# Kernel optimization log

Hardware: AMD Instinct MI355X
Metric: run time of the kernel (lower is better)

Reference implementation:

```python
import math
import jax, jax.numpy as jnp
import numpy as np

B, N, D, H = 4, 2048, 1024, 16
DK = D // H

def setup_inputs() -> dict:
    key = jax.random.key(0)
    k1, k2, k3 = jax.random.split(key, 3)
    x = jax.random.normal(k1, (B, N, D), dtype=jnp.float32)
    # torch Linear weight is [out,in]; we store transposed [in,out] for x @ W
    w_qkv = jax.random.normal(k2, (D, 3 * D), dtype=jnp.float32) * (1.0 / math.sqrt(D))
    w_out = jax.random.normal(k3, (D, D), dtype=jnp.float32) * (1.0 / math.sqrt(D))
    return {"x": x, "w_qkv": w_qkv, "w_out": w_out}

def reference(x, w_qkv, w_out):
    b, n, d = x.shape
    qkv = x @ w_qkv                                   # [B,N,3D]
    q, k, v = jnp.split(qkv, 3, axis=-1)
    def split_heads(t):
        return t.reshape(b, n, H, DK).transpose(0, 2, 1, 3)  # [B,H,N,DK]
    q, k, v = map(split_heads, (q, k, v))
    scale = 1.0 / math.sqrt(DK)
    attn = jnp.einsum('bhqd,bhkd->bhqk', q, k) * scale  # [B,H,N,N]
    attn = jax.nn.softmax(attn, axis=-1)
    out = jnp.einsum('bhqk,bhkd->bhqd', attn, v)        # [B,H,N,DK]
    out = out.transpose(0, 2, 1, 3).reshape(b, n, d)
    return out @ w_out                                  # dropout p=0 -> identity
```

## Files before the change

kernel.cpp:

```cpp
#include <hip/hip_runtime.h>
#include <hip/hip_bf16.h>

typedef __bf16 bf16;
typedef __bf16 bf16x8 __attribute__((ext_vector_type(8)));
typedef float f32x4 __attribute__((ext_vector_type(4)));
typedef float f32x16 __attribute__((ext_vector_type(16)));
typedef short s16x4 __attribute__((ext_vector_type(4)));

#define GLDS16(gp, lp) __builtin_amdgcn_global_load_lds( \
    (const __attribute__((address_space(1))) void*)(gp), \
    (__attribute__((address_space(3))) void*)(lp), 16, 0, 0)

__device__ __forceinline__ bf16 f2bf(float f) {
    unsigned u = __builtin_bit_cast(unsigned, f);
    u = (u + 0x7FFFu + ((u >> 16) & 1u)) >> 16;
    unsigned short s = (unsigned short)u;
    return __builtin_bit_cast(bf16, s);
}
__device__ __forceinline__ void store_c(float* p, float v) { *p = v; }
__device__ __forceinline__ void store_c(bf16*  p, float v) { *p = f2bf(v); }

__device__ __forceinline__ unsigned cvt_pk_bf16(float lo, float hi) {
    unsigned r;
    asm("v_cvt_pk_bf16_f32 %0, %1, %2" : "=v"(r) : "v"(lo), "v"(hi));
    return r;
}
__device__ __forceinline__ void permlane32_swap(unsigned &a, unsigned &b) {
    asm("v_permlane32_swap_b32 %0, %1" : "+v"(a), "+v"(b));
}
__device__ __forceinline__ s16x4 ds_tr16(unsigned addr) {
    s16x4 d;
    asm volatile("ds_read_b64_tr_b16 %0, %1" : "=v"(d) : "v"(addr));
    return d;
}

__global__ __launch_bounds__(256) void cvt_f32_bf16(
    const float* __restrict__ in, bf16* __restrict__ out, int n8)
{
    int i = blockIdx.x * 256 + threadIdx.x;
    if (i >= n8) return;
    f32x4 a = *(const f32x4*)(in + (size_t)i * 8);
    f32x4 b = *(const f32x4*)(in + (size_t)i * 8 + 4);
    bf16x8 o;
    #pragma unroll
    for (int j = 0; j < 4; ++j) { o[j] = f2bf(a[j]); o[4 + j] = f2bf(b[j]); }
    *(bf16x8*)(out + (size_t)i * 8) = o;
}

template <typename TC>
__global__ __launch_bounds__(256) void gemm_glds(
    const bf16* __restrict__ A, const bf16* __restrict__ B, TC* __restrict__ C,
    int M, int N, int K)
{
    __shared__ alignas(16) bf16 As[128 * 32];
    __shared__ alignas(16) bf16 Bs[32 * 128];

    const int tid  = threadIdx.x;
    const int wv   = tid >> 6;
    const int lane = tid & 63;
    const int lr   = lane & 15;
    const int kb   = lane >> 4;
    const int wr   = wv >> 1, wc = wv & 1;
    const int brow = blockIdx.y * 128;
    const int bcol = blockIdx.x * 128;

    f32x4 acc[4][4] = {};

    const int ar0 = wv * 16 + (lane >> 2);
    const int ac0 = (lane & 3) * 8;

    const int bL   = wv * 1024 + lane * 16;
    const int bs0  = bL >> 7;
    const int b_r  = (bL & 127) >> 5;
    const int b_c0 = (bL & 31) >> 1;

    for (int k0 = 0; k0 < K; k0 += 32) {
        __syncthreads();
        #pragma unroll
        for (int t = 0; t < 2; ++t)
            GLDS16(A + (size_t)(brow + t * 64 + ar0) * K + k0 + ac0,
                   &As[t * 2048 + wv * 512]);
        #pragma unroll
        for (int t = 0; t < 2; ++t) {
            int s = bs0 + t * 32;
            GLDS16(B + (size_t)(k0 + (s >> 3) * 4 + b_r) * N + bcol + (s & 7) * 16 + b_c0,
                   &Bs[t * 2048 + wv * 512]);
        }
        __syncthreads();

        bf16x8 af[4], bfr[4];
        #pragma unroll
        for (int m = 0; m < 4; ++m)
            af[m] = *(const bf16x8*)&As[(wr * 64 + m * 16 + lr) * 32 + kb * 8];
        {
            s16x4 tr[8];
            const unsigned bsb = (unsigned)(uintptr_t)Bs + kb * 2048 + lr * 8;
            #pragma unroll
            for (int nt = 0; nt < 4; ++nt) {
                unsigned a = bsb + (wc * 4 + nt) * 128;
                tr[nt * 2]     = ds_tr16(a);
                tr[nt * 2 + 1] = ds_tr16(a + 1024);
            }
            asm volatile("s_waitcnt lgkmcnt(0)" ::: "memory");
            __builtin_amdgcn_sched_barrier(0);
            #pragma unroll
            for (int nt = 0; nt < 4; ++nt) {
                union { bf16x8 f; s16x4 h[2]; } u;
                u.h[0] = tr[nt * 2]; u.h[1] = tr[nt * 2 + 1];
                bfr[nt] = u.f;
            }
        }
        #pragma unroll
        for (int m = 0; m < 4; ++m)
            #pragma unroll
            for (int n = 0; n < 4; ++n)
                acc[m][n] = __builtin_amdgcn_mfma_f32_16x16x32_bf16(af[m], bfr[n], acc[m][n], 0, 0, 0);
    }

    #pragma unroll
    for (int m = 0; m < 4; ++m)
        #pragma unroll
        for (int n = 0; n < 4; ++n)
            #pragma unroll
            for (int r = 0; r < 4; ++r) {
                int row = brow + wr * 64 + m * 16 + kb * 4 + r;
                int col = bcol + wc * 64 + n * 16 + lr;
                store_c(&C[(size_t)row * N + col], acc[m][n][r]);
            }
}

__global__ __launch_bounds__(256) void attn_mfma32(
    const bf16* __restrict__ qkv, bf16* __restrict__ attn_out)
{
    constexpr int NSEQ = 2048, DM = 1024, LD = 3072, KVB = 64, QB = 128;
    __shared__ alignas(16) char smem[18432];
    bf16 (*Ks)[72] = (bf16 (*)[72])smem;
    bf16 *Vs       = (bf16*)(smem + 9216);
    bf16 (*Os)[72] = (bf16 (*)[72])smem;

    const int tid = threadIdx.x;
    const int wv = tid >> 6, lane = tid & 63;
    const int l31 = lane & 31;
    const int hi_ = lane >> 5;
    const int g16 = (lane >> 4) & 1;
    const int l16 = lane & 15;
    const int q0 = blockIdx.x * QB;
    const int bh = blockIdx.y;
    const int b = bh >> 4, h = bh & 15;

    const bf16* qbase = qkv + (size_t)(b * NSEQ) * LD + h * 64;
    const bf16* kbase = qbase + DM;
    const bf16* vbase = qbase + 2 * DM;

    bf16x8 qf[4];
    {
        const bf16* qp = qbase + (size_t)(q0 + wv * 32 + l31) * LD + hi_ * 8;
        #pragma unroll
        for (int ds = 0; ds < 4; ++ds) {
            bf16x8 t = *(const bf16x8*)(qp + ds * 16);
            #pragma unroll
            for (int e = 0; e < 8; ++e) t[e] = f2bf((float)t[e] * 0.125f);
            qf[ds] = t;
        }
    }

    f32x16 o0 = {}, o1 = {};
    float mrow = -INFINITY, lsum = 0.f;

    const int krow = tid >> 2, kcol = (tid & 3) * 16;
    const unsigned vb = (unsigned)(uintptr_t)Vs;

    for (int kt = 0; kt < NSEQ / KVB; ++kt) {
        const int j0 = kt * KVB;
        bf16x8 kr0 = *(const bf16x8*)(kbase + (size_t)(j0 + krow) * LD + kcol);
        bf16x8 kr1 = *(const bf16x8*)(kbase + (size_t)(j0 + krow) * LD + kcol + 8);
        bf16x8 vr[2];
        #pragma unroll
        for (int w = 0; w < 2; ++w) {
            int L = w * 2048 + tid * 8;
            int kq = L >> 8, cb = (L >> 6) & 3, rr = (L >> 4) & 3, c0 = L & 15;
            vr[w] = *(const bf16x8*)(vbase + (size_t)(j0 + kq * 4 + rr) * LD + cb * 16 + c0);
        }
        __syncthreads();
        *(bf16x8*)&Ks[krow][kcol]       = kr0;
        *(bf16x8*)&Ks[krow][kcol + 8]   = kr1;
        *(bf16x8*)(Vs + tid * 8)        = vr[0];
        *(bf16x8*)(Vs + 2048 + tid * 8) = vr[1];
        __syncthreads();

        f32x16 sT0 = {}, sT1 = {};
        #pragma unroll
        for (int ds = 0; ds < 4; ++ds) {
            bf16x8 kf = *(const bf16x8*)&Ks[l31][ds * 16 + hi_ * 8];
            sT0 = __builtin_amdgcn_mfma_f32_32x32x16_bf16(kf, qf[ds], sT0, 0, 0, 0);
        }
        #pragma unroll
        for (int ds = 0; ds < 4; ++ds) {
            bf16x8 kf = *(const bf16x8*)&Ks[32 + l31][ds * 16 + hi_ * 8];
            sT1 = __builtin_amdgcn_mfma_f32_32x32x16_bf16(kf, qf[ds], sT1, 0, 0, 0);
        }

        float pm = sT0[0];
        #pragma unroll
        for (int r = 1; r < 16; ++r) pm = fmaxf(pm, sT0[r]);
        #pragma unroll
        for (int r = 0; r < 16; ++r) pm = fmaxf(pm, sT1[r]);
        pm = fmaxf(pm, __shfl_xor(pm, 32));
        const float mn = fmaxf(mrow, pm);
        const float corr = __expf(mrow - mn);
        mrow = mn;
        float ps = 0.f;
        #pragma unroll
        for (int r = 0; r < 16; ++r) { sT0[r] = __expf(sT0[r] - mn); ps += sT0[r]; }
        #pragma unroll
        for (int r = 0; r < 16; ++r) { sT1[r] = __expf(sT1[r] - mn); ps += sT1[r]; }
        ps += __shfl_xor(ps, 32);
        lsum = lsum * corr + ps;
        #pragma unroll
        for (int r = 0; r < 16; ++r) { o0[r] *= corr; o1[r] *= corr; }

        unsigned w0[8], w1[8];
        #pragma unroll
        for (int j = 0; j < 8; ++j) {
            w0[j] = cvt_pk_bf16(sT0[2 * j], sT0[2 * j + 1]);
            w1[j] = cvt_pk_bf16(sT1[2 * j], sT1[2 * j + 1]);
        }
        bf16x8 pf[4];
        #pragma unroll
        for (int ks = 0; ks < 4; ++ks) {
            const int jb = 4 * (ks & 1);
            unsigned a0 = (ks >> 1) ? w1[jb]     : w0[jb];
            unsigned b0 = (ks >> 1) ? w1[jb + 2] : w0[jb + 2];
            unsigned a1 = (ks >> 1) ? w1[jb + 1] : w0[jb + 1];
            unsigned b1 = (ks >> 1) ? w1[jb + 3] : w0[jb + 3];
            permlane32_swap(a0, b0);
            permlane32_swap(a1, b1);
            union { bf16x8 f; unsigned w[4]; } u;
            u.w[0] = a0; u.w[1] = a1; u.w[2] = b0; u.w[3] = b1;
            pf[ks] = u.f;
        }

        #pragma unroll
        for (int dt = 0; dt < 2; ++dt) {
            s16x4 t[8];
            #pragma unroll
            for (int ks = 0; ks < 4; ++ks) {
                unsigned a = vb + ks * 2048 + hi_ * 1024 + dt * 256 + g16 * 128 + l16 * 8;
                t[ks * 2]     = ds_tr16(a);
                t[ks * 2 + 1] = ds_tr16(a + 512);
            }
            asm volatile("s_waitcnt lgkmcnt(0)" ::: "memory");
            __builtin_amdgcn_sched_barrier(0);
            #pragma unroll
            for (int ks = 0; ks < 4; ++ks) {
                union { bf16x8 f; s16x4 h[2]; } u;
                u.h[0] = t[ks * 2]; u.h[1] = t[ks * 2 + 1];
                if (dt == 0) o0 = __builtin_amdgcn_mfma_f32_32x32x16_bf16(u.f, pf[ks], o0, 0, 0, 0);
                else         o1 = __builtin_amdgcn_mfma_f32_32x32x16_bf16(u.f, pf[ks], o1, 0, 0, 0);
            }
        }
    }

    const float inv = 1.f / lsum;
    __syncthreads();
    #pragma unroll
    for (int r = 0; r < 16; ++r) {
        const int d0 = (r & 3) + 8 * (r >> 2) + 4 * hi_;
        Os[wv * 32 + l31][d0]      = f2bf(o0[r] * inv);
        Os[wv * 32 + l31][32 + d0] = f2bf(o1[r] * inv);
    }
    __syncthreads();
    {
        const int row = tid >> 1, c0 = (tid & 1) * 32;
        bf16* op = attn_out + (size_t)(b * NSEQ + q0 + row) * DM + h * 64 + c0;
        #pragma unroll
        for (int e = 0; e < 4; ++e)
            *(bf16x8*)(op + e * 8) = *(const bf16x8*)&Os[row][c0 + e * 8];
    }
}

extern "C" void kernel_launch(void* const* d_in, const int* in_sizes, int n_in,
                              void* d_out, int out_size, void* d_ws, size_t ws_size,
                              hipStream_t stream) {
    const float* x     = (const float*)d_in[0];
    const float* w_qkv = (const float*)d_in[1];
    const float* w_out = (const float*)d_in[2];
    float* out = (float*)d_out;

    bf16* x_bf    = (bf16*)d_out;
    bf16* qkv     = (bf16*)d_ws;
    bf16* wqkv_bf = qkv + (size_t)8192 * 3072;
    bf16* attnb   = wqkv_bf;
    bf16* wo_bf   = (bf16*)d_ws;

    cvt_f32_bf16<<<4096, 256, 0, stream>>>(x, x_bf, 8192 * 1024 / 8);
    cvt_f32_bf16<<<1536, 256, 0, stream>>>(w_qkv, wqkv_bf, 1024 * 3072 / 8);
    gemm_glds<bf16><<<dim3(3072 / 128, 8192 / 128), 256, 0, stream>>>(
        x_bf, wqkv_bf, qkv, 8192, 3072, 1024);
    attn_mfma32<<<dim3(2048 / 128, 64), 256, 0, stream>>>(qkv, attnb);
    cvt_f32_bf16<<<512, 256, 0, stream>>>(w_out, wo_bf, 1024 * 1024 / 8);
    gemm_glds<float><<<dim3(1024 / 128, 8192 / 128), 256, 0, stream>>>(
        attnb, wo_bf, out, 8192, 1024, 1024);
}
```

Baseline: 240.5 us.

## Prefetch next K/V tile into registers, use exp2 and lazy softmax rescale

The attention kernel now issues global loads for the next K/V tile right after the LDS stores, so they overlap with the current tile's MFMA and softmax work. Q is prescaled by log2(e), which lets the exponentials use the raw v_exp_f32 instruction. The running-max rescale of the accumulators is skipped unless some lane's new max exceeds the old one by more than a threshold. MFMA sections are also bracketed with s_setprio. This trades extra registers for the prefetch and risks bf16 overflow or precision loss from the lazy-rescale threshold.

Result: faster. 220.8 us (-8.2%).

```diff
diff --git a/kernel.cpp b/kernel.cpp
--- a/kernel.cpp
+++ b/kernel.cpp
@@ -20,6 +20,9 @@
 __device__ __forceinline__ void store_c(float* p, float v) { *p = v; }
 __device__ __forceinline__ void store_c(bf16*  p, float v) { *p = f2bf(v); }
 
+__device__ __forceinline__ float exp2_fast(float x) {
+    float r; asm("v_exp_f32 %0, %1" : "=v"(r) : "v"(x)); return r;
+}
 __device__ __forceinline__ unsigned cvt_pk_bf16(float lo, float hi) {
     unsigned r;
     asm("v_cvt_pk_bf16_f32 %0, %1, %2" : "=v"(r) : "v"(lo), "v"(hi));
@@ -133,6 +136,8 @@
     const bf16* __restrict__ qkv, bf16* __restrict__ attn_out)
 {
     constexpr int NSEQ = 2048, DM = 1024, LD = 3072, KVB = 64, QB = 128;
+    constexpr int NT = NSEQ / KVB;
+    constexpr float THR = 11.5f;
     __shared__ alignas(16) char smem[18432];
     bf16 (*Ks)[72] = (bf16 (*)[72])smem;
     bf16 *Vs       = (bf16*)(smem + 9216);
@@ -154,12 +159,13 @@
 
     bf16x8 qf[4];
     {
+        const float QSC = 0.125f * 1.44269504f;
         const bf16* qp = qbase + (size_t)(q0 + wv * 32 + l31) * LD + hi_ * 8;
         #pragma unroll
         for (int ds = 0; ds < 4; ++ds) {
             bf16x8 t = *(const bf16x8*)(qp + ds * 16);
             #pragma unroll
-            for (int e = 0; e < 8; ++e) t[e] = f2bf((float)t[e] * 0.125f);
+            for (int e = 0; e < 8; ++e) t[e] = f2bf((float)t[e] * QSC);
             qf[ds] = t;
         }
     }
@@ -170,25 +176,34 @@
     const int krow = tid >> 2, kcol = (tid & 3) * 16;
     const unsigned vb = (unsigned)(uintptr_t)Vs;
 
-    for (int kt = 0; kt < NSEQ / KVB; ++kt) {
-        const int j0 = kt * KVB;
-        bf16x8 kr0 = *(const bf16x8*)(kbase + (size_t)(j0 + krow) * LD + kcol);
-        bf16x8 kr1 = *(const bf16x8*)(kbase + (size_t)(j0 + krow) * LD + kcol + 8);
-        bf16x8 vr[2];
-        #pragma unroll
-        for (int w = 0; w < 2; ++w) {
-            int L = w * 2048 + tid * 8;
-            int kq = L >> 8, cb = (L >> 6) & 3, rr = (L >> 4) & 3, c0 = L & 15;
-            vr[w] = *(const bf16x8*)(vbase + (size_t)(j0 + kq * 4 + rr) * LD + cb * 16 + c0);
-        }
+    auto vload = [&](int j0, int L) {
+        int kq = L >> 8, cb = (L >> 6) & 3, rr = (L >> 4) & 3, c0 = L & 15;
+        return *(const bf16x8*)(vbase + (size_t)(j0 + kq * 4 + rr) * LD + cb * 16 + c0);
+    };
+
+    bf16x8 kr0 = *(const bf16x8*)(kbase + (size_t)krow * LD + kcol);
+    bf16x8 kr1 = *(const bf16x8*)(kbase + (size_t)krow * LD + kcol + 8);
+    bf16x8 vr0 = vload(0, tid * 8);
+    bf16x8 vr1 = vload(0, 2048 + tid * 8);
+
+    for (int kt = 0; kt < NT; ++kt) {
         __syncthreads();
         *(bf16x8*)&Ks[krow][kcol]       = kr0;
         *(bf16x8*)&Ks[krow][kcol + 8]   = kr1;
-        *(bf16x8*)(Vs + tid * 8)        = vr[0];
-        *(bf16x8*)(Vs + 2048 + tid * 8) = vr[1];
+        *(bf16x8*)(Vs + tid * 8)        = vr0;
+        *(bf16x8*)(Vs + 2048 + tid * 8) = vr1;
         __syncthreads();
 
+        {
+            const int jn = (kt + 1 < NT ? kt + 1 : kt) * KVB;
+            kr0 = *(const bf16x8*)(kbase + (size_t)(jn + krow) * LD + kcol);
+            kr1 = *(const bf16x8*)(kbase + (size_t)(jn + krow) * LD + kcol + 8);
+            vr0 = vload(jn, tid * 8);
+            vr1 = vload(jn, 2048 + tid * 8);
+        }
+
         f32x16 sT0 = {}, sT1 = {};
+        __builtin_amdgcn_s_setprio(1);
         #pragma unroll
         for (int ds = 0; ds < 4; ++ds) {
             bf16x8 kf = *(const bf16x8*)&Ks[l31][ds * 16 + hi_ * 8];
@@ -199,6 +214,7 @@
             bf16x8 kf = *(const bf16x8*)&Ks[32 + l31][ds * 16 + hi_ * 8];
             sT1 = __builtin_amdgcn_mfma_f32_32x32x16_bf16(kf, qf[ds], sT1, 0, 0, 0);
         }
+        __builtin_amdgcn_s_setprio(0);
 
         float pm = sT0[0];
         #pragma unroll
@@ -206,18 +222,21 @@
         #pragma unroll
         for (int r = 0; r < 16; ++r) pm = fmaxf(pm, sT1[r]);
         pm = fmaxf(pm, __shfl_xor(pm, 32));
-        const float mn = fmaxf(mrow, pm);
-        const float corr = __expf(mrow - mn);
-        mrow = mn;
+        if (!__all(pm <= mrow + THR)) {
+            const float mn = fmaxf(mrow, pm);
+            const float corr = exp2_fast(mrow - mn);
+            mrow = mn;
+            lsum *= corr;
+            #pragma unroll
+            for (int r = 0; r < 16; ++r) { o0[r] *= corr; o1[r] *= corr; }
+        }
         float ps = 0.f;
         #pragma unroll
-        for (int r = 0; r < 16; ++r) { sT0[r] = __expf(sT0[r] - mn); ps += sT0[r]; }
-        #pragma unroll
-        for (int r = 0; r < 16; ++r) { sT1[r] = __expf(sT1[r] - mn); ps += sT1[r]; }
+        for (int r = 0; r < 16; ++r) { sT0[r] = exp2_fast(sT0[r] - mrow); ps += sT0[r]; }
+        #pragma unroll
+        for (int r = 0; r < 16; ++r) { sT1[r] = exp2_fast(sT1[r] - mrow); ps += sT1[r]; }
         ps += __shfl_xor(ps, 32);
-        lsum = lsum * corr + ps;
-        #pragma unroll
-        for (int r = 0; r < 16; ++r) { o0[r] *= corr; o1[r] *= corr; }
+        lsum += ps;
 
         unsigned w0[8], w1[8];
         #pragma unroll
@@ -251,6 +270,7 @@
             }
             asm volatile("s_waitcnt lgkmcnt(0)" ::: "memory");
             __builtin_amdgcn_sched_barrier(0);
+            __builtin_amdgcn_s_setprio(1);
             #pragma unroll
             for (int ks = 0; ks < 4; ++ks) {
                 union { bf16x8 f; s16x4 h[2]; } u;
@@ -258,6 +278,7 @@
                 if (dt == 0) o0 = __builtin_amdgcn_mfma_f32_32x32x16_bf16(u.f, pf[ks], o0, 0, 0, 0);
                 else         o1 = __builtin_amdgcn_mfma_f32_32x32x16_bf16(u.f, pf[ks], o1, 0, 0, 0);
             }
+            __builtin_amdgcn_s_setprio(0);
         }
     }
 
```
